# Optimization experiments

Hardware: AMD Instinct MI355X
Metric: run time of the kernel (lower is better)

## Reference

```python
import jax, jax.numpy as jnp
import numpy as np

NF4_LUT = jnp.array([-1.0, -0.6961928009986877, -0.5250730514526367, -0.39491719007492065,
                     -0.28444138169288635, -0.18477343022823334, -0.08820830285549164, 0.0,
                     0.07107656449079514, 0.14263366162776947, 0.22430233657360077,
                     0.3203405737876892, 0.4407068192958832, 0.5905631184577942,
                     0.796090841293335, 1.0], dtype=jnp.float32)

BLOCK_SIZE = 64
OUT_FEATURES = 11008
IN_FEATURES = 4096


def dequantize_nf4(packed, absmax, out_shape):
    # packed: (O, I//2) int codes 0..255; absmax: (O, num_blocks)
    higher = packed // 16
    lower = packed % 16
    unpacked = jnp.stack([lower, higher], axis=-1).reshape(out_shape)  # (O, I)
    dequant = NF4_LUT[unpacked]  # LUT gather -> fp32 (O, I)
    O, I = out_shape
    # block-wise absmax scale
    dequant = (dequant.reshape(O, I // BLOCK_SIZE, BLOCK_SIZE) * absmax[:, :, None]).reshape(O, I)
    return dequant


def setup_inputs() -> dict:
    key = jax.random.key(0)
    k1, k2, k3, k4 = jax.random.split(key, 4)
    x = jax.random.normal(k1, (4, 2048, IN_FEATURES), dtype=jnp.float32)
    weight = jax.random.randint(k2, (OUT_FEATURES, IN_FEATURES // 2), 0, 256, dtype=jnp.int32)
    absmax = jax.random.uniform(k3, (OUT_FEATURES, IN_FEATURES // BLOCK_SIZE), dtype=jnp.float32)
    bias = jax.random.normal(k4, (OUT_FEATURES,), dtype=jnp.float32)
    return {"x": x, "weight": weight, "absmax": absmax, "bias": bias}


def reference(x, weight, absmax, bias):
    w = dequantize_nf4(weight, absmax, (OUT_FEATURES, IN_FEATURES))  # (O, I)
    # F.linear: y = x @ w.T + bias
    return jnp.einsum('bsi,oi->bso', x, w) + bias
```

## Files before the change

### kernel.cpp

```cpp
#include <hip/hip_runtime.h>

#define IN_F 4096
#define OUT_F 11008

typedef __attribute__((ext_vector_type(8))) short bf16x8;
typedef __attribute__((ext_vector_type(4))) float f32x4;
typedef __attribute__((ext_vector_type(4))) unsigned short us4;
typedef __attribute__((ext_vector_type(8))) unsigned short us8;

__device__ __forceinline__ unsigned short f2bf(float f) {
  unsigned int u = __float_as_uint(f);
  u += 0x7FFFu + ((u >> 16) & 1u);
  return (unsigned short)(u >> 16);
}

__global__ __launch_bounds__(256) void cvt_x(const float* __restrict__ X,
                                             unsigned short* __restrict__ Xb, int n8) {
  for (int i = blockIdx.x * blockDim.x + threadIdx.x; i < n8;
       i += gridDim.x * blockDim.x) {
    const float4 a = reinterpret_cast<const float4*>(X)[2 * i];
    const float4 b = reinterpret_cast<const float4*>(X)[2 * i + 1];
    us8 h;
    h[0] = f2bf(a.x); h[1] = f2bf(a.y); h[2] = f2bf(a.z); h[3] = f2bf(a.w);
    h[4] = f2bf(b.x); h[5] = f2bf(b.y); h[6] = f2bf(b.z); h[7] = f2bf(b.w);
    reinterpret_cast<us8*>(Xb)[i] = h;
  }
}

__global__ __launch_bounds__(256) void dequant_w(const int* __restrict__ Wp,
                                                 const float* __restrict__ Amax,
                                                 unsigned short* __restrict__ Wb, int n4) {
  __shared__ float lutS[16];
  if (threadIdx.x < 16) {
    const float lut[16] = {-1.0f, -0.6961928009986877f, -0.5250730514526367f,
        -0.39491719007492065f, -0.28444138169288635f, -0.18477343022823334f,
        -0.08820830285549164f, 0.0f, 0.07107656449079514f, 0.14263366162776947f,
        0.22430233657360077f, 0.3203405737876892f, 0.4407068192958832f,
        0.5905631184577942f, 0.796090841293335f, 1.0f};
    lutS[threadIdx.x] = lut[threadIdx.x];
  }
  __syncthreads();
  for (int i = blockIdx.x * blockDim.x + threadIdx.x; i < n4;
       i += gridDim.x * blockDim.x) {
    const int j = i * 4;
    const int row = j >> 11;
    const int coli = j & 2047;
    const float am = Amax[row * (IN_F / 64) + (coli >> 5)];
    const int4 pk = reinterpret_cast<const int4*>(Wp)[i];
    us8 h; int c;
    c = pk.x & 255; h[0] = f2bf(lutS[c & 15] * am); h[1] = f2bf(lutS[c >> 4] * am);
    c = pk.y & 255; h[2] = f2bf(lutS[c & 15] * am); h[3] = f2bf(lutS[c >> 4] * am);
    c = pk.z & 255; h[4] = f2bf(lutS[c & 15] * am); h[5] = f2bf(lutS[c >> 4] * am);
    c = pk.w & 255; h[6] = f2bf(lutS[c & 15] * am); h[7] = f2bf(lutS[c >> 4] * am);
    reinterpret_cast<us8*>(Wb)[i] = h;
  }
}

#define MF(a, b, c) __builtin_amdgcn_mfma_f32_16x16x32_bf16(a, b, c, 0, 0, 0)
#define GLDS(src, dst) __builtin_amdgcn_global_load_lds( \
    (const __attribute__((address_space(1))) void*)(src), \
    (__attribute__((address_space(3))) void*)(dst), 16, 0, 0)
#define FENCE asm volatile("" ::: "memory")
#define BAR do { FENCE; __builtin_amdgcn_s_barrier(); FENCE; } while (0)
#define VM8 asm volatile("s_waitcnt vmcnt(8)" ::: "memory")
#define VM4 asm volatile("s_waitcnt vmcnt(4)" ::: "memory")
#define VM0 asm volatile("s_waitcnt vmcnt(0)" ::: "memory")
#define VMN do {} while (0)

__global__ __launch_bounds__(512, 2) void gemm256(
    const unsigned short* __restrict__ A,
    const unsigned short* __restrict__ B,
    const float* __restrict__ Bias, float* __restrict__ Out, int M) {
  extern __shared__ unsigned short sm[];
  unsigned short* LA = sm;
  unsigned short* LB = sm + 32768;

  const int tid = threadIdx.x;
  const int l = tid & 63;
  const int wid = tid >> 6;

  const int Mb = M / 256;
  const int Nb = OUT_F / 256;
  const int cpx = (Mb * Nb) >> 3;
  const int bid = (blockIdx.x & 7) * cpx + (blockIdx.x >> 3);
  const int m0 = (bid % Mb) * 256;
  const int n0 = (bid / Mb) * 256;

  const int rh = (l & 15) >> 1;
  const int cph = (((l & 1) << 2) + (l >> 4)) ^ rh;
  const int aoff = (((wid >> 2) * 64) + rh) * 64 + cph * 8;
  const int boff = (((wid & 3) * 32) + rh) * 64 + cph * 8;

  const int cc = (l & 7) ^ (l >> 3);
  const int R0 = 2 * (wid * 16 + (l >> 3)) + (cc >> 2);
  const long chb = (long)(cc & 3) * 16;
  const char* pA0 = (const char*)A + ((size_t)(m0 + R0) * IN_F) * 2 + chb;
  const char* pA1 = (const char*)A + ((size_t)(m0 + R0 + 16) * IN_F) * 2 + chb;
  const char* pB0 = (const char*)B + ((size_t)(n0 + R0) * IN_F) * 2 + chb;
  const char* pB1 = (const char*)B + ((size_t)(n0 + R0 + 16) * IN_F) * 2 + chb;
  const int dq0 = wid * 1024;
  const int dq1 = wid * 1024 + 512;

#define STAGE_A(tt) do { const int s_ = ((tt) & 3) * 8192; const size_t ko_ = (size_t)(tt) * 64; \
    GLDS(pA0 + ko_, LA + s_ + dq0); GLDS(pA1 + ko_, LA + s_ + dq1); } while (0)
#define STAGE_B(tt) do { const int s_ = ((tt) & 3) * 8192; const size_t ko_ = (size_t)(tt) * 64; \
    GLDS(pB0 + ko_, LB + s_ + dq0); GLDS(pB1 + ko_, LB + s_ + dq1); } while (0)

  f32x4 acc[8][4];
#pragma unroll
  for (int i = 0; i < 8; ++i)
#pragma unroll
    for (int j = 0; j < 4; ++j) acc[i][j] = {0.f, 0.f, 0.f, 0.f};

  STAGE_A(0); STAGE_B(0); STAGE_A(1); STAGE_B(1); STAGE_A(2); STAGE_B(2);
  VM8;
  __builtin_amdgcn_s_barrier();
  FENCE;

#define TILE(t, STG, VMW) do { \
  const int sb = ((t) & 3) * 8192; \
  bf16x8 a0, a1, a2, a3, b0, b1, b2, b3; \
  a0 = *(const bf16x8*)(LA + sb + aoff); \
  a1 = *(const bf16x8*)(LA + sb + aoff + 512); \
  a2 = *(const bf16x8*)(LA + sb + aoff + 1024); \
  a3 = *(const bf16x8*)(LA + sb + aoff + 1536); \
  b0 = *(const bf16x8*)(LB + sb + boff); \
  b1 = *(const bf16x8*)(LB + sb + boff + 512); \
  b2 = *(const bf16x8*)(LB + sb + boff + 1024); \
  b3 = *(const bf16x8*)(LB + sb + boff + 1536); \
  if (STG) STAGE_A((t) + 3); \
  BAR; \
  __builtin_amdgcn_s_setprio(1); \
  acc[0][0] = MF(a0, b0, acc[0][0]); acc[0][1] = MF(a0, b1, acc[0][1]); \
  acc[0][2] = MF(a0, b2, acc[0][2]); acc[0][3] = MF(a0, b3, acc[0][3]); \
  acc[1][0] = MF(a1, b0, acc[1][0]); acc[1][1] = MF(a1, b1, acc[1][1]); \
  acc[1][2] = MF(a1, b2, acc[1][2]); acc[1][3] = MF(a1, b3, acc[1][3]); \
  acc[2][0] = MF(a2, b0, acc[2][0]); acc[2][1] = MF(a2, b1, acc[2][1]); \
  acc[2][2] = MF(a2, b2, acc[2][2]); acc[2][3] = MF(a2, b3, acc[2][3]); \
  acc[3][0] = MF(a3, b0, acc[3][0]); acc[3][1] = MF(a3, b1, acc[3][1]); \
  acc[3][2] = MF(a3, b2, acc[3][2]); acc[3][3] = MF(a3, b3, acc[3][3]); \
  __builtin_amdgcn_s_setprio(0); \
  BAR; \
  a0 = *(const bf16x8*)(LA + sb + aoff + 2048); \
  a1 = *(const bf16x8*)(LA + sb + aoff + 2560); \
  a2 = *(const bf16x8*)(LA + sb + aoff + 3072); \
  a3 = *(const bf16x8*)(LA + sb + aoff + 3584); \
  if (STG) STAGE_B((t) + 3); \
  BAR; \
  __builtin_amdgcn_s_setprio(1); \
  acc[4][0] = MF(a0, b0, acc[4][0]); acc[4][1] = MF(a0, b1, acc[4][1]); \
  acc[4][2] = MF(a0, b2, acc[4][2]); acc[4][3] = MF(a0, b3, acc[4][3]); \
  acc[5][0] = MF(a1, b0, acc[5][0]); acc[5][1] = MF(a1, b1, acc[5][1]); \
  acc[5][2] = MF(a1, b2, acc[5][2]); acc[5][3] = MF(a1, b3, acc[5][3]); \
  acc[6][0] = MF(a2, b0, acc[6][0]); acc[6][1] = MF(a2, b1, acc[6][1]); \
  acc[6][2] = MF(a2, b2, acc[6][2]); acc[6][3] = MF(a2, b3, acc[6][3]); \
  acc[7][0] = MF(a3, b0, acc[7][0]); acc[7][1] = MF(a3, b1, acc[7][1]); \
  acc[7][2] = MF(a3, b2, acc[7][2]); acc[7][3] = MF(a3, b3, acc[7][3]); \
  __builtin_amdgcn_s_setprio(0); \
  VMW; \
  BAR; \
} while (0)

  for (int t = 0; t < 125; ++t) { TILE(t, 1, VM8); }
  TILE(125, 0, VM4);
  TILE(126, 0, VM0);
  TILE(127, 0, VMN);

  const int crow = m0 + (wid >> 2) * 128 + ((l >> 4) << 2);
  const int ccol = n0 + (wid & 3) * 64 + (l & 15);
#pragma unroll
  for (int nf = 0; nf < 4; ++nf) {
    const float bv = Bias[ccol + nf * 16];
#pragma unroll
    for (int f = 0; f < 8; ++f)
#pragma unroll
      for (int rg = 0; rg < 4; ++rg)
        Out[(size_t)(crow + f * 16 + rg) * OUT_F + ccol + nf * 16] = acc[f][nf][rg] + bv;
  }
}

__global__ __launch_bounds__(256, 2) void nf4_gemm_fused(
    const float* __restrict__ X, const int* __restrict__ Wp,
    const float* __restrict__ Amax, const float* __restrict__ Bias,
    float* __restrict__ Out, int M) {
  __shared__ unsigned short As[128 * 64];
  __shared__ unsigned short Bs[128 * 64];
  __shared__ float lutS[16];

  const int t = threadIdx.x;
  const int l = t & 63;
  const int wid = t >> 6;

  if (t < 16) {
    const float lut[16] = {-1.0f, -0.6961928009986877f, -0.5250730514526367f,
        -0.39491719007492065f, -0.28444138169288635f, -0.18477343022823334f,
        -0.08820830285549164f, 0.0f, 0.07107656449079514f, 0.14263366162776947f,
        0.22430233657360077f, 0.3203405737876892f, 0.4407068192958832f,
        0.5905631184577942f, 0.796090841293335f, 1.0f};
    lutS[t] = lut[t];
  }

  const int ntile = OUT_F / 128;
  const int m0 = (blockIdx.x / ntile) * 128;
  const int n0 = (blockIdx.x % ntile) * 128;

  const int ar = t >> 4;
  const int ac4 = t & 15;
  const int br = t >> 3;
  const int bg = t & 7;
  const int wm = (wid >> 1) * 64;
  const int wn = (wid & 1) * 64;

  f32x4 acc[4][4];
#pragma unroll
  for (int i = 0; i < 4; ++i)
#pragma unroll
    for (int j = 0; j < 4; ++j) acc[i][j] = {0.f, 0.f, 0.f, 0.f};

  __syncthreads();

  for (int k0 = 0; k0 < IN_F; k0 += 64) {
#pragma unroll
    for (int p = 0; p < 8; ++p) {
      const int r = p * 16 + ar;
      const float4 v = *reinterpret_cast<const float4*>(
          X + (size_t)(m0 + r) * IN_F + k0 + ac4 * 4);
      us4 h;
      h[0] = f2bf(v.x); h[1] = f2bf(v.y); h[2] = f2bf(v.z); h[3] = f2bf(v.w);
      const int byte = r * 128 + ((ac4 * 8) ^ ((r & 7) << 4));
      *reinterpret_cast<us4*>(reinterpret_cast<char*>(As) + byte) = h;
    }
#pragma unroll
    for (int p = 0; p < 4; ++p) {
      const int r = p * 32 + br;
      const float amv = Amax[(size_t)(n0 + r) * (IN_F / 64) + (k0 >> 6)];
      const int4 pk = *reinterpret_cast<const int4*>(
          Wp + (size_t)(n0 + r) * (IN_F / 2) + (k0 >> 1) + bg * 4);
      us8 h;
      {
        int c;
        c = pk.x & 255; h[0] = f2bf(lutS[c & 15] * amv); h[1] = f2bf(lutS[c >> 4] * amv);
        c = pk.y & 255; h[2] = f2bf(lutS[c & 15] * amv); h[3] = f2bf(lutS[c >> 4] * amv);
        c = pk.z & 255; h[4] = f2bf(lutS[c & 15] * amv); h[5] = f2bf(lutS[c >> 4] * amv);
        c = pk.w & 255; h[6] = f2bf(lutS[c & 15] * amv); h[7] = f2bf(lutS[c >> 4] * amv);
      }
      const int byte = r * 128 + ((bg * 16) ^ ((r & 7) << 4));
      *reinterpret_cast<us8*>(reinterpret_cast<char*>(Bs) + byte) = h;
    }
    __syncthreads();

#pragma unroll
    for (int kk = 0; kk < 64; kk += 32) {
      bf16x8 af[4], bfv[4];
      const int kb = (kk + ((l >> 4) << 3)) * 2;
#pragma unroll
      for (int i = 0; i < 4; ++i) {
        const int row = wm + i * 16 + (l & 15);
        af[i] = *reinterpret_cast<const bf16x8*>(
            reinterpret_cast<const char*>(As) + row * 128 + (kb ^ ((row & 7) << 4)));
      }
#pragma unroll
      for (int j = 0; j < 4; ++j) {
        const int row = wn + j * 16 + (l & 15);
        bfv[j] = *reinterpret_cast<const bf16x8*>(
            reinterpret_cast<const char*>(Bs) + row * 128 + (kb ^ ((row & 7) << 4)));
      }
#pragma unroll
      for (int i = 0; i < 4; ++i)
#pragma unroll
        for (int j = 0; j < 4; ++j)
          acc[i][j] = __builtin_amdgcn_mfma_f32_16x16x32_bf16(af[i], bfv[j], acc[i][j], 0, 0, 0);
    }
    __syncthreads();
  }

  const int crow0 = m0 + wm + ((l >> 4) << 2);
  const int ccol0 = n0 + wn + (l & 15);
#pragma unroll
  for (int j = 0; j < 4; ++j) {
    const float bv = Bias[ccol0 + j * 16];
#pragma unroll
    for (int i = 0; i < 4; ++i)
#pragma unroll
      for (int rg = 0; rg < 4; ++rg)
        Out[(size_t)(crow0 + i * 16 + rg) * OUT_F + ccol0 + j * 16] = acc[i][j][rg] + bv;
  }
}

extern "C" void kernel_launch(void* const* d_in, const int* in_sizes, int n_in,
                              void* d_out, int out_size, void* d_ws, size_t ws_size,
                              hipStream_t stream) {
  const float* X = (const float*)d_in[0];
  const int* Wp = (const int*)d_in[1];
  const float* Amax = (const float*)d_in[2];
  const float* Bias = (const float*)d_in[3];
  float* Out = (float*)d_out;

  const int M = in_sizes[0] / IN_F;
  const size_t needX = (size_t)M * IN_F * 2;
  const size_t needW = (size_t)OUT_F * IN_F * 2;
  const int grid256 = (M / 256) * (OUT_F / 256);

  if (ws_size >= needX + needW && (M % 256) == 0 && (grid256 & 7) == 0) {
    unsigned short* Xb = (unsigned short*)d_ws;
    unsigned short* Wb = Xb + (size_t)M * IN_F;
    (void)hipFuncSetAttribute(reinterpret_cast<const void*>(gemm256),
                              hipFuncAttributeMaxDynamicSharedMemorySize, 131072);
    cvt_x<<<2048, 256, 0, stream>>>(X, Xb, M * (IN_F / 8));
    dequant_w<<<2048, 256, 0, stream>>>(Wp, Amax, Wb, OUT_F * (IN_F / 8));
    gemm256<<<grid256, 512, 131072, stream>>>(Xb, Wb, Bias, Out, M);
  } else {
    const int grid = (M / 128) * (OUT_F / 128);
    nf4_gemm_fused<<<grid, 256, 0, stream>>>(X, Wp, Amax, Bias, Out, M);
  }
}
```

Measured before the change: 896.2 us.

## Restructure GEMM main loop to use a single barrier per K-tile

The bf16 GEMM main loop is reorganised so that each K-tile begins with one vmcnt wait plus a barrier, instead of four barriers spread through the tile. All eight A fragments and four B fragments are read from LDS up front, and both the A and B prefetches for tile t+3 are issued together between the two MFMA halves. The prologue wait is folded into the loop, and the tail wait counts are shifted to match. This cuts barrier stalls and gives each wave a longer stretch of uninterrupted MFMA work, at the cost of extra VGPRs for the additional A fragments.

```diff
diff --git a/kernel.cpp b/kernel.cpp
--- a/kernel.cpp
+++ b/kernel.cpp
@@ -65,7 +65,6 @@
 #define VM8 asm volatile("s_waitcnt vmcnt(8)" ::: "memory")
 #define VM4 asm volatile("s_waitcnt vmcnt(4)" ::: "memory")
 #define VM0 asm volatile("s_waitcnt vmcnt(0)" ::: "memory")
-#define VMN do {} while (0)
 
 __global__ __launch_bounds__(512, 2) void gemm256(
     const unsigned short* __restrict__ A,
@@ -113,13 +112,12 @@
     for (int j = 0; j < 4; ++j) acc[i][j] = {0.f, 0.f, 0.f, 0.f};
 
   STAGE_A(0); STAGE_B(0); STAGE_A(1); STAGE_B(1); STAGE_A(2); STAGE_B(2);
-  VM8;
-  __builtin_amdgcn_s_barrier();
-  FENCE;
 
 #define TILE(t, STG, VMW) do { \
+  VMW; \
+  BAR; \
   const int sb = ((t) & 3) * 8192; \
-  bf16x8 a0, a1, a2, a3, b0, b1, b2, b3; \
+  bf16x8 a0, a1, a2, a3, a4, a5, a6, a7, b0, b1, b2, b3; \
   a0 = *(const bf16x8*)(LA + sb + aoff); \
   a1 = *(const bf16x8*)(LA + sb + aoff + 512); \
   a2 = *(const bf16x8*)(LA + sb + aoff + 1024); \
@@ -128,8 +126,10 @@
   b1 = *(const bf16x8*)(LB + sb + boff + 512); \
   b2 = *(const bf16x8*)(LB + sb + boff + 1024); \
   b3 = *(const bf16x8*)(LB + sb + boff + 1536); \
-  if (STG) STAGE_A((t) + 3); \
-  BAR; \
+  a4 = *(const bf16x8*)(LA + sb + aoff + 2048); \
+  a5 = *(const bf16x8*)(LA + sb + aoff + 2560); \
+  a6 = *(const bf16x8*)(LA + sb + aoff + 3072); \
+  a7 = *(const bf16x8*)(LA + sb + aoff + 3584); \
   __builtin_amdgcn_s_setprio(1); \
   acc[0][0] = MF(a0, b0, acc[0][0]); acc[0][1] = MF(a0, b1, acc[0][1]); \
   acc[0][2] = MF(a0, b2, acc[0][2]); acc[0][3] = MF(a0, b3, acc[0][3]); \
@@ -140,31 +140,23 @@
   acc[3][0] = MF(a3, b0, acc[3][0]); acc[3][1] = MF(a3, b1, acc[3][1]); \
   acc[3][2] = MF(a3, b2, acc[3][2]); acc[3][3] = MF(a3, b3, acc[3][3]); \
   __builtin_amdgcn_s_setprio(0); \
-  BAR; \
-  a0 = *(const bf16x8*)(LA + sb + aoff + 2048); \
-  a1 = *(const bf16x8*)(LA + sb + aoff + 2560); \
-  a2 = *(const bf16x8*)(LA + sb + aoff + 3072); \
-  a3 = *(const bf16x8*)(LA + sb + aoff + 3584); \
-  if (STG) STAGE_B((t) + 3); \
-  BAR; \
+  if (STG) { STAGE_A((t) + 3); STAGE_B((t) + 3); } \
   __builtin_amdgcn_s_setprio(1); \
-  acc[4][0] = MF(a0, b0, acc[4][0]); acc[4][1] = MF(a0, b1, acc[4][1]); \
-  acc[4][2] = MF(a0, b2, acc[4][2]); acc[4][3] = MF(a0, b3, acc[4][3]); \
-  acc[5][0] = MF(a1, b0, acc[5][0]); acc[5][1] = MF(a1, b1, acc[5][1]); \
-  acc[5][2] = MF(a1, b2, acc[5][2]); acc[5][3] = MF(a1, b3, acc[5][3]); \
-  acc[6][0] = MF(a2, b0, acc[6][0]); acc[6][1] = MF(a2, b1, acc[6][1]); \
-  acc[6][2] = MF(a2, b2, acc[6][2]); acc[6][3] = MF(a2, b3, acc[6][3]); \
-  acc[7][0] = MF(a3, b0, acc[7][0]); acc[7][1] = MF(a3, b1, acc[7][1]); \
-  acc[7][2] = MF(a3, b2, acc[7][2]); acc[7][3] = MF(a3, b3, acc[7][3]); \
+  acc[4][0] = MF(a4, b0, acc[4][0]); acc[4][1] = MF(a4, b1, acc[4][1]); \
+  acc[4][2] = MF(a4, b2, acc[4][2]); acc[4][3] = MF(a4, b3, acc[4][3]); \
+  acc[5][0] = MF(a5, b0, acc[5][0]); acc[5][1] = MF(a5, b1, acc[5][1]); \
+  acc[5][2] = MF(a5, b2, acc[5][2]); acc[5][3] = MF(a5, b3, acc[5][3]); \
+  acc[6][0] = MF(a6, b0, acc[6][0]); acc[6][1] = MF(a6, b1, acc[6][1]); \
+  acc[6][2] = MF(a6, b2, acc[6][2]); acc[6][3] = MF(a6, b3, acc[6][3]); \
+  acc[7][0] = MF(a7, b0, acc[7][0]); acc[7][1] = MF(a7, b1, acc[7][1]); \
+  acc[7][2] = MF(a7, b2, acc[7][2]); acc[7][3] = MF(a7, b3, acc[7][3]); \
   __builtin_amdgcn_s_setprio(0); \
-  VMW; \
-  BAR; \
 } while (0)
 
   for (int t = 0; t < 125; ++t) { TILE(t, 1, VM8); }
-  TILE(125, 0, VM4);
-  TILE(126, 0, VM0);
-  TILE(127, 0, VMN);
+  TILE(125, 0, VM8);
+  TILE(126, 0, VM4);
+  TILE(127, 0, VM0);
 
   const int crow = m0 + (wid >> 2) * 128 + ((l >> 4) << 2);
   const int ccol = n0 + (wid & 3) * 64 + (l & 15);
```

After: 850.4 us. 1.05x faster.
